# Kernel tuning notes

Hardware: AMD Instinct MI355X
Metric: run time of the kernel (lower is better)

The kernel has to match this reference:

```python
import jax, jax.numpy as jnp
import numpy as np

N = 100000   # nodes
E = 1600000  # edges
D = 128      # input_dim == hidden_dim
OUT = 64     # output_dim
G = 64       # graphs in batch
L = 4        # GIN layers = num_layers - 1
BN_EPS = 1e-5


def setup_inputs() -> dict:
    key = jax.random.key(0)
    ks = jax.random.split(key, 16)
    inp = {
        "h": jax.random.normal(ks[0], (N, D), dtype=jnp.float32),
        "efeat": jnp.zeros((1,), dtype=jnp.float32),
        "src": jax.random.randint(ks[1], (E,), 0, N, dtype=jnp.int32),
        "dst": jax.random.randint(ks[2], (E,), 0, N, dtype=jnp.int32),
        "graph_id": jnp.sort(jax.random.randint(ks[3], (N,), 0, G, dtype=jnp.int32)),
        # learnable eps per GIN layer (init 0, as GINConv(init_eps=0))
        "eps": jnp.zeros((L,), dtype=jnp.float32),
        # 2-layer MLP per GIN layer
        "mlp_W1": jax.random.normal(ks[4], (L, D, D), dtype=jnp.float32) / np.sqrt(D),
        "mlp_b1": jnp.zeros((L, D), dtype=jnp.float32),
        "mlp_W2": jax.random.normal(ks[5], (L, D, D), dtype=jnp.float32) / np.sqrt(D),
        "mlp_b2": jnp.zeros((L, D), dtype=jnp.float32),
        # BN inside MLP (after first linear)
        "mlp_bn_g": jnp.ones((L, D), dtype=jnp.float32),
        "mlp_bn_b": jnp.zeros((L, D), dtype=jnp.float32),
        # BN of ApplyNodeFunc
        "apply_bn_g": jnp.ones((L, D), dtype=jnp.float32),
        "apply_bn_b": jnp.zeros((L, D), dtype=jnp.float32),
        # outer per-layer BN in UnsupervisedGIN
        "outer_bn_g": jnp.ones((L, D), dtype=jnp.float32),
        "outer_bn_b": jnp.zeros((L, D), dtype=jnp.float32),
        # prediction heads: layer 0 on input (D) + L heads on hidden (D)
        "pred_W": jax.random.normal(ks[6], (L + 1, D, OUT), dtype=jnp.float32) / np.sqrt(D),
        "pred_b": jnp.zeros((L + 1, OUT), dtype=jnp.float32),
    }
    return inp


def _bn(x, g, b):
    # train-mode BatchNorm1d over node axis
    m = x.mean(axis=0)
    v = x.var(axis=0)
    return (x - m) * jax.lax.rsqrt(v + BN_EPS) * g + b


def reference(h, efeat, src, dst, graph_id, eps,
              mlp_W1, mlp_b1, mlp_W2, mlp_b2,
              mlp_bn_g, mlp_bn_b, apply_bn_g, apply_bn_b,
              outer_bn_g, outer_bn_b, pred_W, pred_b):
    hidden_rep = [h]
    for i in range(L):
        # GINConv, neighbor_pooling = sum: aggregate src features into dst
        agg = jax.ops.segment_sum(h[src], dst, num_segments=N)  # [N, D]
        x = (1.0 + eps[i]) * h + agg
        # ApplyNodeFunc: MLP(2 layers) -> BN -> ReLU
        z = jax.nn.relu(_bn(x @ mlp_W1[i] + mlp_b1[i], mlp_bn_g[i], mlp_bn_b[i]))
        z = z @ mlp_W2[i] + mlp_b2[i]
        z = jax.nn.relu(_bn(z, apply_bn_g[i], apply_bn_b[i]))
        # outer BN + ReLU
        h = jax.nn.relu(_bn(z, outer_bn_g[i], outer_bn_b[i]))
        hidden_rep.append(h)

    # SumPooling per layer + prediction heads (dropout = identity at eval)
    pooled = [jax.ops.segment_sum(hh, graph_id, num_segments=G) for hh in hidden_rep]
    score = sum(p @ pred_W[i] + pred_b[i] for i, p in enumerate(pooled))  # [G, OUT]
    return (score, tuple(pooled[1:]))
```

## Files before the change

### kernel.cpp

```cpp
#include <hip/hip_runtime.h>

constexpr int D   = 128;
constexpr int G   = 64;
constexpr int OUT = 64;
constexpr int L   = 4;
#define BN_EPS 1e-5f

constexpr int BSH    = 9;
constexpr int BNODES = 1 << BSH;
constexpr int SC_CHUNK = 8192;

typedef __attribute__((ext_vector_type(8))) short bf16x8;
typedef __attribute__((ext_vector_type(4))) short short4v;
typedef __attribute__((ext_vector_type(4))) float f32x4;
typedef unsigned short u16;

__device__ inline u16 f2bf(float f) {
    union { float f; unsigned u; } x; x.f = f;
    unsigned r = x.u + 0x7FFF + ((x.u >> 16) & 1);
    return (u16)(r >> 16);
}
__device__ inline float bf2f(u16 u) {
    union { unsigned u; float f; } x; x.u = ((unsigned)u) << 16;
    return x.f;
}

__global__ __launch_bounds__(256) void bucket_hist(const int* __restrict__ dst,
                                                   int* __restrict__ bktCnt,
                                                   int nE, int numB) {
    __shared__ int h[4096];
    const int tid = threadIdx.x;
    for (int i = tid; i < numB; i += 256) h[i] = 0;
    __syncthreads();
    const int stride = gridDim.x * 256;
    for (int e = blockIdx.x * 256 + tid; e < nE; e += stride)
        atomicAdd(&h[dst[e] >> BSH], 1);
    __syncthreads();
    for (int i = tid; i < numB; i += 256)
        if (h[i]) atomicAdd(&bktCnt[i], h[i]);
}

__global__ __launch_bounds__(256) void scan_buckets(const int* __restrict__ bktCnt,
                                                    int* __restrict__ bktOff,
                                                    int* __restrict__ bktCur,
                                                    int numB, int total) {
    __shared__ int sm[256];
    const int tid = threadIdx.x;
    int v[4];
    int s = 0;
#pragma unroll
    for (int j = 0; j < 4; ++j) {
        int i = tid * 4 + j;
        v[j] = (i < numB) ? bktCnt[i] : 0;
        s += v[j];
    }
    sm[tid] = s;
    __syncthreads();
    for (int off = 1; off < 256; off <<= 1) {
        int t = (tid >= off) ? sm[tid - off] : 0;
        __syncthreads();
        sm[tid] += t;
        __syncthreads();
    }
    int run = sm[tid] - s;
#pragma unroll
    for (int j = 0; j < 4; ++j) {
        int i = tid * 4 + j;
        if (i < numB) { bktOff[i] = run; bktCur[i] = run; }
        run += v[j];
    }
    if (tid == 0) bktOff[numB] = total;
}

__global__ __launch_bounds__(256) void bucket_scatter(const int* __restrict__ src,
                                                      const int* __restrict__ dst,
                                                      int* __restrict__ bktCur,
                                                      int2* __restrict__ sorted,
                                                      int nE, int numB) {
    __shared__ int h[1024];
    __shared__ int base[1024];
    const int tid = threadIdx.x;
    const int lo = blockIdx.x * SC_CHUNK;
    const int hi = min(lo + SC_CHUNK, nE);
    for (int i = tid; i < numB; i += 256) h[i] = 0;
    __syncthreads();
    for (int e = lo + tid; e < hi; e += 256)
        atomicAdd(&h[dst[e] >> BSH], 1);
    __syncthreads();
    for (int i = tid; i < numB; i += 256) {
        int c = h[i];
        base[i] = c ? atomicAdd(&bktCur[i], c) : 0;
        h[i] = 0;
    }
    __syncthreads();
    for (int e = lo + tid; e < hi; e += 256) {
        int d = dst[e];
        int b = d >> BSH;
        int pos = base[b] + atomicAdd(&h[b], 1);
        sorted[pos] = make_int2(src[e], d);
    }
}

__global__ __launch_bounds__(256) void bucket_deg(const int2* __restrict__ sorted,
                                                  const int* __restrict__ bktOff,
                                                  int* __restrict__ deg, int nN) {
    __shared__ int h[BNODES];
    const int tid = threadIdx.x;
    const int b = blockIdx.x;
    for (int j = tid; j < BNODES; j += 256) h[j] = 0;
    __syncthreads();
    const int lo = bktOff[b], hi = bktOff[b + 1];
    for (int i = lo + tid; i < hi; i += 256)
        atomicAdd(&h[sorted[i].y & (BNODES - 1)], 1);
    __syncthreads();
    const int node0 = b << BSH;
    for (int j = tid; j < BNODES; j += 256) {
        int n = node0 + j;
        if (n < nN) deg[n] = h[j];
    }
}

__global__ __launch_bounds__(256) void csr_fill2(const int2* __restrict__ sorted,
                                                 const int* __restrict__ bktOff,
                                                 const int* __restrict__ rowptr,
                                                 int* __restrict__ esrc, int nN) {
    __shared__ int cur[BNODES];
    const int tid = threadIdx.x;
    const int b = blockIdx.x;
    const int node0 = b << BSH;
    for (int j = tid; j < BNODES; j += 256) {
        int n = node0 + j;
        cur[j] = (n < nN) ? rowptr[n] : 0;
    }
    __syncthreads();
    const int lo = bktOff[b], hi = bktOff[b + 1];
    for (int i = lo + tid; i < hi; i += 256) {
        int2 e = sorted[i];
        int pos = atomicAdd(&cur[e.y & (BNODES - 1)], 1);
        esrc[pos] = e.x;
    }
}

constexpr int SCAN_B = 256;
constexpr int SCAN_E = 8;
constexpr int SCAN_CHUNK = SCAN_B * SCAN_E;

__global__ __launch_bounds__(SCAN_B) void scan_pass1(const int* __restrict__ deg,
                                                     int* __restrict__ rowptr,
                                                     int* __restrict__ bsum, int n) {
    __shared__ int sm[SCAN_B];
    const int tid = threadIdx.x;
    const int base = blockIdx.x * SCAN_CHUNK + tid * SCAN_E;
    int v[SCAN_E];
    int s = 0;
#pragma unroll
    for (int j = 0; j < SCAN_E; ++j) {
        v[j] = (base + j < n) ? deg[base + j] : 0;
        s += v[j];
    }
    sm[tid] = s;
    __syncthreads();
    for (int off = 1; off < SCAN_B; off <<= 1) {
        int t = (tid >= off) ? sm[tid - off] : 0;
        __syncthreads();
        sm[tid] += t;
        __syncthreads();
    }
    int run = sm[tid] - s;
#pragma unroll
    for (int j = 0; j < SCAN_E; ++j) {
        if (base + j < n) rowptr[base + j] = run;
        run += v[j];
    }
    if (tid == SCAN_B - 1) bsum[blockIdx.x] = sm[SCAN_B - 1];
}

__global__ void scan_pass2(int* __restrict__ bsum, int nb) {
    if (threadIdx.x == 0 && blockIdx.x == 0) {
        int t = 0;
        for (int i = 0; i < nb; ++i) {
            int s = bsum[i];
            bsum[i] = t;
            t += s;
        }
    }
}

__global__ __launch_bounds__(SCAN_B) void scan_pass3(int* __restrict__ rowptr,
                                                     const int* __restrict__ bsum,
                                                     int n, int total) {
    const int add = bsum[blockIdx.x];
    const int base = blockIdx.x * SCAN_CHUNK + threadIdx.x * SCAN_E;
#pragma unroll
    for (int j = 0; j < SCAN_E; ++j)
        if (base + j < n) rowptr[base + j] += add;
    if (blockIdx.x == 0 && threadIdx.x == 0) rowptr[n] = total;
}

__global__ void prep_weights(const float* __restrict__ W1, const float* __restrict__ W2,
                             u16* __restrict__ Wt) {
    const int m = blockIdx.x;
    const float* W = (m < L) ? (W1 + (size_t)m * D * D) : (W2 + (size_t)(m - L) * D * D);
    u16* o = Wt + (size_t)m * D * D;
    for (int e = threadIdx.x * 4; e < D * D; e += 256 * 4) {
        float4 v = *reinterpret_cast<const float4*>(W + e);
        int k = e >> 7, c = e & 127;
        o[(c + 0) * D + k] = f2bf(v.x);
        o[(c + 1) * D + k] = f2bf(v.y);
        o[(c + 2) * D + k] = f2bf(v.z);
        o[(c + 3) * D + k] = f2bf(v.w);
    }
}

__global__ __launch_bounds__(256) void convert_pool(const float* __restrict__ h, const int* __restrict__ gid,
                                                    u16* __restrict__ hbf, float* __restrict__ pooled,
                                                    int nRows) {
    const int tid = threadIdx.x;
    const int c = tid & 127;
    const int rsub = tid >> 7;
    const long long row0 = (long long)blockIdx.x * 64;
    float acc = 0.f;
    int cur = -1;
    for (int r = rsub; r < 64; r += 2) {
        long long row = row0 + r;
        if (row >= nRows) break;
        float v = h[row * D + c];
        hbf[row * D + c] = f2bf(v);
        int g = gid[row];
        if (g != cur) {
            if (cur >= 0) atomicAdd(&pooled[(long long)cur * D + c], acc);
            cur = g;
            acc = 0.f;
        }
        acc += v;
    }
    if (cur >= 0) atomicAdd(&pooled[(long long)cur * D + c], acc);
}

__global__ __launch_bounds__(256) void agg_gather(const u16* __restrict__ hbf,
                                                  const int* __restrict__ rowptr,
                                                  const int* __restrict__ esrc,
                                                  const float* __restrict__ epsP,
                                                  u16* __restrict__ xbf, int nRows) {
    const int r = blockIdx.x * 16 + (threadIdx.x >> 4);
    if (r >= nRows) return;
    const int c = (threadIdx.x & 15) * 8;
    const int beg = rowptr[r], end = rowptr[r + 1];
    const float ep = 1.0f + epsP[0];
    bf16x8 a = *reinterpret_cast<const bf16x8*>(hbf + (size_t)r * D + c);
    float acc[8];
#pragma unroll
    for (int j = 0; j < 8; ++j) acc[j] = ep * bf2f((u16)a[j]);

    int e = beg;
    for (; e + 8 <= end; e += 8) {
        bf16x8 v[8];
#pragma unroll
        for (int q = 0; q < 8; ++q) {
            int s = esrc[e + q];
            v[q] = *reinterpret_cast<const bf16x8*>(hbf + (size_t)s * D + c);
        }
#pragma unroll
        for (int j = 0; j < 8; ++j) {
            float t0 = (bf2f((u16)v[0][j]) + bf2f((u16)v[1][j])) + (bf2f((u16)v[2][j]) + bf2f((u16)v[3][j]));
            float t1 = (bf2f((u16)v[4][j]) + bf2f((u16)v[5][j])) + (bf2f((u16)v[6][j]) + bf2f((u16)v[7][j]));
            acc[j] += t0 + t1;
        }
    }
    for (; e + 4 <= end; e += 4) {
        bf16x8 v[4];
#pragma unroll
        for (int q = 0; q < 4; ++q) {
            int s = esrc[e + q];
            v[q] = *reinterpret_cast<const bf16x8*>(hbf + (size_t)s * D + c);
        }
#pragma unroll
        for (int j = 0; j < 8; ++j)
            acc[j] += (bf2f((u16)v[0][j]) + bf2f((u16)v[1][j])) + (bf2f((u16)v[2][j]) + bf2f((u16)v[3][j]));
    }
    for (; e < end; ++e) {
        int s = esrc[e];
        bf16x8 v = *reinterpret_cast<const bf16x8*>(hbf + (size_t)s * D + c);
#pragma unroll
        for (int j = 0; j < 8; ++j) acc[j] += bf2f((u16)v[j]);
    }
    bf16x8 o;
#pragma unroll
    for (int j = 0; j < 8; ++j) o[j] = (short)f2bf(acc[j]);
    *reinterpret_cast<bf16x8*>(xbf + (size_t)r * D + c) = o;
}

template <int MODE>
__global__ __launch_bounds__(256) void gemm_mfma(
    const u16* __restrict__ A, const u16* __restrict__ Wt, const float* __restrict__ bias,
    const float* __restrict__ pSum, const float* __restrict__ pSq,
    const float* __restrict__ bng, const float* __restrict__ bnb, float invN,
    u16* __restrict__ outP, float* __restrict__ gsum, float* __restrict__ gsq,
    int nRows) {
    __shared__ u16 wL[D * D];
    __shared__ float redS[D], redQ[D];
    __shared__ float scL[D], shL[D];

    const int tid = threadIdx.x;
    const int row0 = blockIdx.x * 128;
    const int lane = tid & 63;
    const int wv = tid >> 6;
    const int wrow = wv * 32;
    const int lr = lane & 15;
    const int lb = lane >> 4;

    bf16x8 aR[2][4];
    bool valid[2];
#pragma unroll
    for (int m = 0; m < 2; ++m) {
        int row = row0 + wrow + m * 16 + lr;
        valid[m] = row < nRows;
        const u16* p = A + (size_t)(valid[m] ? row : (nRows - 1)) * D + lb * 8;
#pragma unroll
        for (int kk = 0; kk < 4; ++kk)
            aR[m][kk] = *reinterpret_cast<const bf16x8*>(p + kk * 32);
    }

    for (int o = tid * 8; o < D * D; o += 2048) {
        bf16x8 v = *reinterpret_cast<const bf16x8*>(Wt + o);
        int byte = o * 2, r = byte >> 8;
        *reinterpret_cast<bf16x8*>((char*)wL + (byte ^ ((r & 7) << 4))) = v;
    }
    if (tid < D) {
        redS[tid] = 0.f; redQ[tid] = 0.f;
        if (MODE == 1) {
            float m = pSum[tid] * invN;
            float v = pSq[tid] * invN - m * m;
            float sc = bng[tid] * rsqrtf(v + BN_EPS);
            scL[tid] = sc;
            shL[tid] = bnb[tid] - m * sc;
        }
    }
    __syncthreads();

    if (MODE == 1) {
#pragma unroll
        for (int m = 0; m < 2; ++m)
#pragma unroll
            for (int kk = 0; kk < 4; ++kk)
#pragma unroll
                for (int j = 0; j < 8; ++j) {
                    int c = kk * 32 + lb * 8 + j;
                    float t = fmaxf(bf2f((u16)aR[m][kk][j]) * scL[c] + shL[c], 0.f);
                    aR[m][kk][j] = (short)f2bf(t);
                }
    }
#pragma unroll
    for (int m = 0; m < 2; ++m)
        if (!valid[m])
#pragma unroll
            for (int kk = 0; kk < 4; ++kk) aR[m][kk] = bf16x8{};

    f32x4 acc[2][8] = {};
#pragma unroll
    for (int kk = 0; kk < 4; ++kk) {
#pragma unroll
        for (int n = 0; n < 8; ++n) {
            int cr = n * 16 + lr;
            int byte = cr * 256 + kk * 64 + lb * 16;
            bf16x8 bF = *reinterpret_cast<const bf16x8*>((char*)wL + (byte ^ ((cr & 7) << 4)));
            acc[0][n] = __builtin_amdgcn_mfma_f32_16x16x32_bf16(aR[0][kk], bF, acc[0][n], 0, 0, 0);
            acc[1][n] = __builtin_amdgcn_mfma_f32_16x16x32_bf16(aR[1][kk], bF, acc[1][n], 0, 0, 0);
        }
    }

    float ls[8], lq[8];
#pragma unroll
    for (int n = 0; n < 8; ++n) { ls[n] = 0.f; lq[n] = 0.f; }
#pragma unroll
    for (int n = 0; n < 8; ++n) {
        int col = n * 16 + lr;
        float bv = bias[col];
#pragma unroll
        for (int m = 0; m < 2; ++m) {
#pragma unroll
            for (int j = 0; j < 4; ++j) {
                int row = row0 + wrow + m * 16 + lb * 4 + j;
                if (row < nRows) {
                    float o = acc[m][n][j] + bv;
                    outP[(size_t)row * D + col] = f2bf(o);
                    ls[n] += o; lq[n] += o * o;
                }
            }
        }
    }
#pragma unroll
    for (int n = 0; n < 8; ++n) {
        float s = ls[n], q = lq[n];
        s += __shfl_xor(s, 16); q += __shfl_xor(q, 16);
        s += __shfl_xor(s, 32); q += __shfl_xor(q, 32);
        if (lb == 0) {
            atomicAdd(&redS[n * 16 + lr], s);
            atomicAdd(&redQ[n * 16 + lr], q);
        }
    }
    __syncthreads();
    if (tid < D) {
        atomicAdd(&gsum[tid], redS[tid]);
        atomicAdd(&gsq[tid], redQ[tid]);
    }
}

__global__ __launch_bounds__(256) void relu_bn_stats(const u16* __restrict__ z,
                                                     const float* __restrict__ pSum, const float* __restrict__ pSq,
                                                     const float* __restrict__ bng, const float* __restrict__ bnb,
                                                     float invN,
                                                     float* __restrict__ gsum, float* __restrict__ gsq,
                                                     long long n8) {
    __shared__ float redS[D], redQ[D];
    const int tid = threadIdx.x;
    if (tid < D) { redS[tid] = 0.f; redQ[tid] = 0.f; }
    __syncthreads();
    const int c = (tid & 15) * 8;
    float sc[8], sh[8];
#pragma unroll
    for (int j = 0; j < 8; ++j) {
        float m = pSum[c + j] * invN;
        float v = pSq[c + j] * invN - m * m;
        float s = bng[c + j] * rsqrtf(v + BN_EPS);
        sc[j] = s;
        sh[j] = bnb[c + j] - m * s;
    }
    const long long stride = (long long)gridDim.x * blockDim.x;
    float ls[8] = {}, lq[8] = {};
    for (long long i = (long long)blockIdx.x * blockDim.x + tid; i < n8; i += stride) {
        bf16x8 v = *reinterpret_cast<const bf16x8*>(z + i * 8);
#pragma unroll
        for (int j = 0; j < 8; ++j) {
            float t = fmaxf(bf2f((u16)v[j]) * sc[j] + sh[j], 0.f);
            ls[j] += t; lq[j] += t * t;
        }
    }
#pragma unroll
    for (int j = 0; j < 8; ++j) {
        atomicAdd(&redS[c + j], ls[j]);
        atomicAdd(&redQ[c + j], lq[j]);
    }
    __syncthreads();
    if (tid < D) {
        atomicAdd(&gsum[tid], redS[tid]);
        atomicAdd(&gsq[tid], redQ[tid]);
    }
}

__global__ __launch_bounds__(256) void final_apply_pool(
    const u16* __restrict__ z, const int* __restrict__ gid,
    const float* __restrict__ p1S, const float* __restrict__ p1Q,
    const float* __restrict__ g2, const float* __restrict__ b2v,
    const float* __restrict__ p2S, const float* __restrict__ p2Q,
    const float* __restrict__ g3, const float* __restrict__ b3v,
    float invN, u16* __restrict__ hbf, float* __restrict__ pooled, int nRows) {
    const int tid = threadIdx.x;
    const int c = tid & 127;
    const int rsub = tid >> 7;
    const long long row0 = (long long)blockIdx.x * 64;

    float m = p1S[c] * invN;
    float va = p1Q[c] * invN - m * m;
    float a2 = g2[c] * rsqrtf(va + BN_EPS);
    float f2v = b2v[c] - m * a2;
    m = p2S[c] * invN;
    va = p2Q[c] * invN - m * m;
    float a3 = g3[c] * rsqrtf(va + BN_EPS);
    float f3v = b3v[c] - m * a3;

    float acc = 0.f;
    int cur = -1;
    for (int r = rsub; r < 64; r += 2) {
        long long row = row0 + r;
        if (row >= nRows) break;
        float v = bf2f(z[row * D + c]);
        v = fmaxf(fmaxf(v * a2 + f2v, 0.f) * a3 + f3v, 0.f);
        hbf[row * D + c] = f2bf(v);
        int g = gid[row];
        if (g != cur) {
            if (cur >= 0) atomicAdd(&pooled[(long long)cur * D + c], acc);
            cur = g;
            acc = 0.f;
        }
        acc += v;
    }
    if (cur >= 0) atomicAdd(&pooled[(long long)cur * D + c], acc);
}

__global__ __launch_bounds__(256) void pred_heads(const float* __restrict__ pooled0,
                                                  const float* __restrict__ pooledL,
                                                  const float* __restrict__ pW,
                                                  const float* __restrict__ pb,
                                                  float* __restrict__ score) {
    __shared__ float red[256];
    __shared__ float pL[D];
    const int g = blockIdx.x;
    const int o = threadIdx.x & 63;
    const int ks = threadIdx.x >> 6;
    float acc = 0.f;
    for (int i = 0; i <= L; ++i) {
        const float* p = (i == 0) ? (pooled0 + (size_t)g * D)
                                  : (pooledL + (size_t)(i - 1) * G * D + (size_t)g * D);
        if (threadIdx.x < D) pL[threadIdx.x] = p[threadIdx.x];
        __syncthreads();
        const float* w = pW + (size_t)i * D * OUT + (size_t)ks * 32 * OUT + o;
        float s = 0.f;
#pragma unroll
        for (int kk = 0; kk < 32; ++kk)
            s += pL[ks * 32 + kk] * w[kk * OUT];
        acc += s;
        if (ks == 0) acc += pb[i * OUT + o];
        __syncthreads();
    }
    red[threadIdx.x] = acc;
    __syncthreads();
    if (ks == 0)
        score[(size_t)g * OUT + o] = red[o] + red[64 + o] + red[128 + o] + red[192 + o];
}

extern "C" void kernel_launch(void* const* d_in, const int* in_sizes, int n_in,
                              void* d_out, int out_size, void* d_ws, size_t ws_size,
                              hipStream_t stream) {
    const float* h0  = (const float*)d_in[0];
    const int*   src = (const int*)d_in[2];
    const int*   dst = (const int*)d_in[3];
    const int*   gid = (const int*)d_in[4];
    const float* eps = (const float*)d_in[5];
    const float* W1  = (const float*)d_in[6];
    const float* b1  = (const float*)d_in[7];
    const float* W2  = (const float*)d_in[8];
    const float* b2  = (const float*)d_in[9];
    const float* bn1g = (const float*)d_in[10];
    const float* bn1b = (const float*)d_in[11];
    const float* bn2g = (const float*)d_in[12];
    const float* bn2b = (const float*)d_in[13];
    const float* bn3g = (const float*)d_in[14];
    const float* bn3b = (const float*)d_in[15];
    const float* pW  = (const float*)d_in[16];
    const float* pb  = (const float*)d_in[17];

    const int N = in_sizes[0] / D;
    const int E = in_sizes[2];
    const size_t nd = (size_t)N * D;
    const int numB = (N + BNODES - 1) >> BSH;

    u16*   hbf  = (u16*)d_ws;
    u16*   xbf  = hbf + nd;
    u16*   Wt   = xbf + nd;
    float* stats = (float*)(Wt + (size_t)2 * L * D * D);
    float* pooled0 = stats + (size_t)L * 3 * 2 * D;
    int*   bktCnt = (int*)(pooled0 + (size_t)G * D);
    int*   bktOff = bktCnt + 4096;
    int*   bktCur = bktOff + 4096;
    int*   deg    = bktCur + 4096;
    int*   rowptr = deg + N;
    int*   esrc   = rowptr + (N + 1);
    int*   bsum   = esrc + E;
    int2*  sorted = (int2*)(((size_t)(bsum + 4096) + 15) & ~(size_t)15);

    float* score = (float*)d_out;
    float* pooledOut = score + G * OUT;

    auto S = [&](int i, int j) { return stats + (size_t)(i * 3 + j) * 2 * D; };
    auto Q = [&](int i, int j) { return stats + (size_t)(i * 3 + j) * 2 * D + D; };

    const int nb = (N + SCAN_CHUNK - 1) / SCAN_CHUNK;
    const int sgrid = (E + SC_CHUNK - 1) / SC_CHUNK;
    const int hgrid = (E + 2047) / 2048;
    const int poolGrid = (N + 63) / 64;
    const int ggrid = (N + 127) / 128;
    const int agrid = (N + 15) / 16;
    const long long n8 = (long long)N * (D / 8);
    const float invN = 1.0f / (float)N;

    const size_t zeroBytes = ((size_t)L * 3 * 2 * D + (size_t)G * D) * sizeof(float) + 4096 * sizeof(int);
    hipMemsetAsync(stats, 0, zeroBytes, stream);
    hipMemsetAsync(d_out, 0, (size_t)out_size * sizeof(float), stream);

    bucket_hist<<<hgrid, 256, 0, stream>>>(dst, bktCnt, E, numB);
    prep_weights<<<2 * L, 256, 0, stream>>>(W1, W2, Wt);
    scan_buckets<<<1, 256, 0, stream>>>(bktCnt, bktOff, bktCur, numB, E);
    bucket_scatter<<<sgrid, 256, 0, stream>>>(src, dst, bktCur, sorted, E, numB);
    bucket_deg<<<numB, 256, 0, stream>>>(sorted, bktOff, deg, N);
    scan_pass1<<<nb, SCAN_B, 0, stream>>>(deg, rowptr, bsum, N);
    scan_pass2<<<1, 64, 0, stream>>>(bsum, nb);
    scan_pass3<<<nb, SCAN_B, 0, stream>>>(rowptr, bsum, N, E);
    csr_fill2<<<numB, 256, 0, stream>>>(sorted, bktOff, rowptr, esrc, N);

    convert_pool<<<poolGrid, 256, 0, stream>>>(h0, gid, hbf, pooled0, N);

    for (int i = 0; i < L; ++i) {
        agg_gather<<<agrid, 256, 0, stream>>>(hbf, rowptr, esrc, eps + i, xbf, N);

        gemm_mfma<2><<<ggrid, 256, 0, stream>>>(
            xbf, Wt + (size_t)i * D * D, b1 + (size_t)i * D,
            nullptr, nullptr, nullptr, nullptr, invN,
            xbf, S(i, 0), Q(i, 0), N);

        gemm_mfma<1><<<ggrid, 256, 0, stream>>>(
            xbf, Wt + (size_t)(L + i) * D * D, b2 + (size_t)i * D,
            S(i, 0), Q(i, 0), bn1g + (size_t)i * D, bn1b + (size_t)i * D, invN,
            xbf, S(i, 1), Q(i, 1), N);

        relu_bn_stats<<<1024, 256, 0, stream>>>(
            xbf, S(i, 1), Q(i, 1), bn2g + (size_t)i * D, bn2b + (size_t)i * D, invN,
            S(i, 2), Q(i, 2), n8);

        final_apply_pool<<<poolGrid, 256, 0, stream>>>(
            xbf, gid,
            S(i, 1), Q(i, 1), bn2g + (size_t)i * D, bn2b + (size_t)i * D,
            S(i, 2), Q(i, 2), bn3g + (size_t)i * D, bn3b + (size_t)i * D,
            invN, hbf, pooledOut + (size_t)i * G * D, N);
    }

    pred_heads<<<G, 256, 0, stream>>>(pooled0, pooledOut, pW, pb, score);
}
```

Before: 953.7 us.

## Pack sorted edges into single int and stage GEMM output through LDS

Packs each bucket-sorted edge into one 32-bit word: the source id in the low 17 bits and the destination's offset within its bucket in the high bits. This halves the traffic of the intermediate sorted array across scatter, degree and CSR fill. Separately, the GEMM epilogue now writes bf16 results into a padded LDS tile, then stores full rows to global memory with 16-byte vector stores instead of scattered 2-byte stores. This costs a larger shared-memory footprint (which may lower occupancy) and an extra barrier, and it assumes N fits in 17 bits.

```diff
diff --git a/kernel.cpp b/kernel.cpp
--- a/kernel.cpp
+++ b/kernel.cpp
@@ -9,6 +9,8 @@
 constexpr int BSH    = 9;
 constexpr int BNODES = 1 << BSH;
 constexpr int SC_CHUNK = 8192;
+constexpr int SRC_BITS = 17;
+constexpr int SRC_MASK = (1 << SRC_BITS) - 1;
 
 typedef __attribute__((ext_vector_type(8))) short bf16x8;
 typedef __attribute__((ext_vector_type(4))) short short4v;
@@ -75,7 +77,7 @@
 __global__ __launch_bounds__(256) void bucket_scatter(const int* __restrict__ src,
                                                       const int* __restrict__ dst,
                                                       int* __restrict__ bktCur,
-                                                      int2* __restrict__ sorted,
+                                                      int* __restrict__ sorted,
                                                       int nE, int numB) {
     __shared__ int h[1024];
     __shared__ int base[1024];
@@ -97,11 +99,11 @@
         int d = dst[e];
         int b = d >> BSH;
         int pos = base[b] + atomicAdd(&h[b], 1);
-        sorted[pos] = make_int2(src[e], d);
-    }
-}
-
-__global__ __launch_bounds__(256) void bucket_deg(const int2* __restrict__ sorted,
+        sorted[pos] = src[e] | ((d & (BNODES - 1)) << SRC_BITS);
+    }
+}
+
+__global__ __launch_bounds__(256) void bucket_deg(const int* __restrict__ sorted,
                                                   const int* __restrict__ bktOff,
                                                   int* __restrict__ deg, int nN) {
     __shared__ int h[BNODES];
@@ -111,7 +113,7 @@
     __syncthreads();
     const int lo = bktOff[b], hi = bktOff[b + 1];
     for (int i = lo + tid; i < hi; i += 256)
-        atomicAdd(&h[sorted[i].y & (BNODES - 1)], 1);
+        atomicAdd(&h[(sorted[i] >> SRC_BITS) & (BNODES - 1)], 1);
     __syncthreads();
     const int node0 = b << BSH;
     for (int j = tid; j < BNODES; j += 256) {
@@ -120,7 +122,7 @@
     }
 }
 
-__global__ __launch_bounds__(256) void csr_fill2(const int2* __restrict__ sorted,
+__global__ __launch_bounds__(256) void csr_fill2(const int* __restrict__ sorted,
                                                  const int* __restrict__ bktOff,
                                                  const int* __restrict__ rowptr,
                                                  int* __restrict__ esrc, int nN) {
@@ -135,9 +137,9 @@
     __syncthreads();
     const int lo = bktOff[b], hi = bktOff[b + 1];
     for (int i = lo + tid; i < hi; i += 256) {
-        int2 e = sorted[i];
-        int pos = atomicAdd(&cur[e.y & (BNODES - 1)], 1);
-        esrc[pos] = e.x;
+        int p = sorted[i];
+        int pos = atomicAdd(&cur[(p >> SRC_BITS) & (BNODES - 1)], 1);
+        esrc[pos] = p & SRC_MASK;
     }
 }
 
@@ -290,6 +292,8 @@
     *reinterpret_cast<bf16x8*>(xbf + (size_t)r * D + c) = o;
 }
 
+constexpr int CSTRIDE = D + 8;
+
 template <int MODE>
 __global__ __launch_bounds__(256) void gemm_mfma(
     const u16* __restrict__ A, const u16* __restrict__ Wt, const float* __restrict__ bias,
@@ -297,7 +301,7 @@
     const float* __restrict__ bng, const float* __restrict__ bnb, float invN,
     u16* __restrict__ outP, float* __restrict__ gsum, float* __restrict__ gsq,
     int nRows) {
-    __shared__ u16 wL[D * D];
+    __shared__ u16 wLx[D * CSTRIDE];
     __shared__ float redS[D], redQ[D];
     __shared__ float scL[D], shL[D];
 
@@ -324,7 +328,7 @@
     for (int o = tid * 8; o < D * D; o += 2048) {
         bf16x8 v = *reinterpret_cast<const bf16x8*>(Wt + o);
         int byte = o * 2, r = byte >> 8;
-        *reinterpret_cast<bf16x8*>((char*)wL + (byte ^ ((r & 7) << 4))) = v;
+        *reinterpret_cast<bf16x8*>((char*)wLx + (byte ^ ((r & 7) << 4))) = v;
     }
     if (tid < D) {
         redS[tid] = 0.f; redQ[tid] = 0.f;
@@ -363,11 +367,12 @@
         for (int n = 0; n < 8; ++n) {
             int cr = n * 16 + lr;
             int byte = cr * 256 + kk * 64 + lb * 16;
-            bf16x8 bF = *reinterpret_cast<const bf16x8*>((char*)wL + (byte ^ ((cr & 7) << 4)));
+            bf16x8 bF = *reinterpret_cast<const bf16x8*>((char*)wLx + (byte ^ ((cr & 7) << 4)));
             acc[0][n] = __builtin_amdgcn_mfma_f32_16x16x32_bf16(aR[0][kk], bF, acc[0][n], 0, 0, 0);
             acc[1][n] = __builtin_amdgcn_mfma_f32_16x16x32_bf16(aR[1][kk], bF, acc[1][n], 0, 0, 0);
         }
     }
+    __syncthreads();
 
     float ls[8], lq[8];
 #pragma unroll
@@ -380,12 +385,10 @@
         for (int m = 0; m < 2; ++m) {
 #pragma unroll
             for (int j = 0; j < 4; ++j) {
-                int row = row0 + wrow + m * 16 + lb * 4 + j;
-                if (row < nRows) {
-                    float o = acc[m][n][j] + bv;
-                    outP[(size_t)row * D + col] = f2bf(o);
-                    ls[n] += o; lq[n] += o * o;
-                }
+                int rloc = wrow + m * 16 + lb * 4 + j;
+                float o = acc[m][n][j] + bv;
+                wLx[rloc * CSTRIDE + col] = f2bf(o);
+                if (row0 + rloc < nRows) { ls[n] += o; lq[n] += o * o; }
             }
         }
     }
@@ -400,6 +403,20 @@
         }
     }
     __syncthreads();
+
+    {
+        int rloc = tid >> 1;
+        int row = row0 + rloc;
+        if (row < nRows) {
+            const int c0 = (tid & 1) * 64;
+            const u16* srcL = wLx + rloc * CSTRIDE + c0;
+            u16* dstG = outP + (size_t)row * D + c0;
+#pragma unroll
+            for (int q = 0; q < 8; ++q)
+                *reinterpret_cast<bf16x8*>(dstG + q * 8) =
+                    *reinterpret_cast<const bf16x8*>(srcL + q * 8);
+        }
+    }
     if (tid < D) {
         atomicAdd(&gsum[tid], redS[tid]);
         atomicAdd(&gsq[tid], redQ[tid]);
@@ -557,7 +574,7 @@
     int*   rowptr = deg + N;
     int*   esrc   = rowptr + (N + 1);
     int*   bsum   = esrc + E;
-    int2*  sorted = (int2*)(((size_t)(bsum + 4096) + 15) & ~(size_t)15);
+    int*   sorted = bsum + 4096;
 
     float* score = (float*)d_out;
     float* pooledOut = score + G * OUT;
```

Measured after the change: 875.6 us (median of 2 runs). -8.2%, faster.
